# Performance work log

Hardware: AMD Instinct MI355X
Metric: run time of the kernel (lower is better)

The kernel has to match this reference:

```python
import jax, jax.numpy as jnp
import numpy as np

VOCAB = 33
V2 = VOCAB * VOCAB  # 1089
BUCKETS = 512


def setup_inputs() -> dict:
    key = jax.random.key(0)
    ks = jax.random.split(key, 9)
    B, S = 4096, 4096
    src = jax.random.randint(ks[0], (B, S), 0, VOCAB, dtype=jnp.int64 if jax.config.jax_enable_x64 else jnp.int32)
    def lin(k, fan_in, fan_out):
        bound = 1.0 / np.sqrt(fan_in)
        return jax.random.uniform(k, (fan_in, fan_out), jnp.float32, -bound, bound)
    return {
        "src": src,
        "Wb1": lin(ks[1], V2, 256), "bb1": jax.random.normal(ks[2], (256,), jnp.float32) * 0.01,
        "Wb2": lin(ks[3], 256, 32), "bb2": jax.random.normal(ks[4], (32,), jnp.float32) * 0.01,
        "Wt1": lin(ks[5], BUCKETS, 256), "bt1": jax.random.normal(ks[6], (256,), jnp.float32) * 0.01,
        "Wt2": lin(ks[7], 256, 32), "bt2": jax.random.normal(ks[8], (32,), jnp.float32) * 0.01,
    }


def _hist_freqs(indices, mask, n_bins):
    # indices: [B, L] int, mask: [B, L] bool -> normalized per-row histogram [B, n_bins]
    B = indices.shape[0]
    rows = jnp.arange(B)[:, None]
    counts = jnp.zeros((B, n_bins), jnp.float32).at[rows, indices].add(mask.astype(jnp.float32))
    lens = jnp.clip(mask.sum(axis=1, keepdims=True).astype(jnp.float32), 1.0, None)
    return counts / lens


def reference(src, Wb1, bb1, Wb2, bb2, Wt1, bt1, Wt2, bt2):
    # bigram histogram
    cur, nxt = src[:, :-1], src[:, 1:]
    bi_idx = cur * VOCAB + nxt
    bi_mask = (cur > 0) & (nxt > 0)
    bi_freq = _hist_freqs(bi_idx, bi_mask, V2)
    bi_feat = jax.nn.relu(bi_freq @ Wb1 + bb1) @ Wb2 + bb2
    # trigram hashed histogram
    c1, c2, c3 = src[:, :-2], src[:, 1:-1], src[:, 2:]
    tri_idx = (c1 * (VOCAB * VOCAB) + c2 * VOCAB + c3) % BUCKETS
    tri_mask = (c1 > 0) & (c2 > 0) & (c3 > 0)
    tri_freq = _hist_freqs(tri_idx, tri_mask, BUCKETS)
    tri_feat = jax.nn.relu(tri_freq @ Wt1 + bt1) @ Wt2 + bt2
    return jnp.concatenate([bi_feat, tri_feat], axis=1)  # [B, 64]
```

## Files before the change

kernel.cpp:

```cpp
#include <hip/hip_runtime.h>
#include <hip/hip_bf16.h>

#define TOK_S    4096
#define NBI      1089
#define NBI_P    1092
#define KP_BI    1120
#define NTRI     512
#define NHID     256
#define NROWS    4096
#define HSTRIDE  (NHID + 4)

#define HIST_BLKS   (NROWS / 2)
#define TRANS_ELEMS (NHID * KP_BI + NHID * NTRI)
#define TRANS_BLKS  (TRANS_ELEMS / 1024)

typedef __attribute__((ext_vector_type(8))) short short8;
typedef __attribute__((ext_vector_type(4))) float f32x4;

__global__ __launch_bounds__(256)
void hist_trans(const int* __restrict__ src,
                const float* __restrict__ Wb1, const float* __restrict__ Wt1,
                __hip_bfloat16* __restrict__ Abi,
                __hip_bfloat16* __restrict__ Atri,
                __hip_bfloat16* __restrict__ WbT,
                __hip_bfloat16* __restrict__ WtT,
                float* __restrict__ inv)
{
    __shared__ int   s_bi [2][NBI_P];
    __shared__ int   s_tri[2][NTRI];
    __shared__ float s_ps [2][2][2];

    const int tid = threadIdx.x;

    if (blockIdx.x >= HIST_BLKS) {
        int base = (blockIdx.x - HIST_BLKS) * 1024 + tid;
        const int nb = NHID * KP_BI;
        #pragma unroll
        for (int i = 0; i < 4; ++i) {
            int idx = base + i * 256;
            if (idx < nb) {
                int c = idx / KP_BI, k = idx - c * KP_BI;
                WbT[idx] = __float2bfloat16(k < NBI ? Wb1[k * NHID + c] : 0.0f);
            } else {
                int j = idx - nb;
                int c = j >> 9, k = j & 511;
                WtT[j] = __float2bfloat16(Wt1[k * NHID + c]);
            }
        }
        return;
    }

    const int wave = tid >> 6;
    const int lane = tid & 63;
    const int wrow = wave >> 1;
    const int wpar = wave & 1;
    const size_t row = (size_t)blockIdx.x * 2 + wrow;

    for (int i = tid; i < 2 * NBI_P; i += 256) ((int*)s_bi)[i]  = 0;
    for (int i = tid; i < 2 * NTRI;  i += 256) ((int*)s_tri)[i] = 0;
    __syncthreads();

    int* bi  = s_bi[wrow];
    int* tri = s_tri[wrow];
    const int4* rowp = (const int4*)(src + row * TOK_S);
    const int*  rowt = src + row * TOK_S;

    #pragma unroll
    for (int j = 0; j < 8; ++j) {
        const int idx = wpar * 512 + j * 64 + lane;
        int4 c = rowp[idx];
        int e0 = 0, e1 = 0;
        if (idx != 1023) {
            const int2 e = *(const int2*)(rowt + idx * 4 + 4);
            e0 = e.x; e1 = e.y;
        }
        const bool mx = c.x > 0, my = c.y > 0, mz = c.z > 0, mw = c.w > 0;
        const bool m4 = e0 > 0, m5 = e1 > 0;
        const int b0 = c.x * 33 + c.y;
        const int b1 = c.y * 33 + c.z;
        const int b2 = c.z * 33 + c.w;
        const int b3 = c.w * 33 + e0;
        if (mx & my) atomicAdd(&bi[b0], 1);
        if (my & mz) atomicAdd(&bi[b1], 1);
        if (mz & mw) atomicAdd(&bi[b2], 1);
        if (mw & m4) atomicAdd(&bi[b3], 1);
        if (mx & my & mz) atomicAdd(&tri[(b0 * 33 + c.z) & 511], 1);
        if (my & mz & mw) atomicAdd(&tri[(b1 * 33 + c.w) & 511], 1);
        if (mz & mw & m4) atomicAdd(&tri[(b2 * 33 + e0) & 511], 1);
        if (mw & m4 & m5) atomicAdd(&tri[(b3 * 33 + e1) & 511], 1);
    }
    __syncthreads();

    float bsum = 0.0f, tsum = 0.0f;
    __hip_bfloat16* arow = Abi + row * KP_BI;
    for (int i = wpar * 64 + lane; i < KP_BI; i += 128) {
        float f = (i < NBI) ? (float)bi[i] : 0.0f;
        bsum += f;
        arow[i] = __float2bfloat16(f);
    }
    __hip_bfloat16* trow = Atri + row * NTRI;
    for (int i = wpar * 64 + lane; i < NTRI; i += 128) {
        float f = (float)tri[i];
        tsum += f;
        trow[i] = __float2bfloat16(f);
    }
    #pragma unroll
    for (int s = 32; s; s >>= 1) {
        bsum += __shfl_xor(bsum, s, 64);
        tsum += __shfl_xor(tsum, s, 64);
    }
    if (lane == 0) { s_ps[wrow][wpar][0] = bsum; s_ps[wrow][wpar][1] = tsum; }
    __syncthreads();
    if (tid < 2) {
        float bs = s_ps[tid][0][0] + s_ps[tid][1][0];
        float ts = s_ps[tid][0][1] + s_ps[tid][1][1];
        size_t r2 = ((size_t)blockIdx.x * 2 + tid) * 2;
        inv[r2 + 0] = 1.0f / fmaxf(bs, 1.0f);
        inv[r2 + 1] = 1.0f / fmaxf(ts, 1.0f);
    }
}

template<int KP>
__device__ __forceinline__
void head_body(const __hip_bfloat16* __restrict__ A,
               const __hip_bfloat16* __restrict__ WT,
               const float* __restrict__ b1,
               const float* __restrict__ W2,
               const float* __restrict__ b2,
               const float* __restrict__ inv, const int invoff, const int headoff,
               float* __restrict__ out, const int m0,
               float (*sH)[HSTRIDE])
{
    const int wave = threadIdx.x >> 6;
    const int lane = threadIdx.x & 63;
    const int wn   = wave * 32;
    const int fr   = lane & 15;
    const int kg   = lane >> 4;

    const __hip_bfloat16* A0 = A  + (size_t)(m0 + fr) * KP + kg * 8;
    const __hip_bfloat16* A1 = A0 + (size_t)16 * KP;
    const __hip_bfloat16* B0 = WT + (size_t)(wn + fr) * KP + kg * 8;
    const __hip_bfloat16* B1 = B0 + (size_t)16 * KP;

    f32x4 acc00 = {}, acc01 = {}, acc10 = {}, acc11 = {};
    #pragma unroll 4
    for (int k = 0; k < KP; k += 32) {
        short8 a0  = *(const short8*)(A0 + k);
        short8 a1  = *(const short8*)(A1 + k);
        short8 b0  = *(const short8*)(B0 + k);
        short8 b1v = *(const short8*)(B1 + k);
        acc00 = __builtin_amdgcn_mfma_f32_16x16x32_bf16(a0, b0,  acc00, 0, 0, 0);
        acc01 = __builtin_amdgcn_mfma_f32_16x16x32_bf16(a0, b1v, acc01, 0, 0, 0);
        acc10 = __builtin_amdgcn_mfma_f32_16x16x32_bf16(a1, b0,  acc10, 0, 0, 0);
        acc11 = __builtin_amdgcn_mfma_f32_16x16x32_bf16(a1, b1v, acc11, 0, 0, 0);
    }

    f32x4 accs[2][2] = { {acc00, acc01}, {acc10, acc11} };
    #pragma unroll
    for (int mf = 0; mf < 2; ++mf) {
        #pragma unroll
        for (int nf = 0; nf < 2; ++nf) {
            const int col = wn + nf * 16 + fr;
            const float bias = b1[col];
            #pragma unroll
            for (int r = 0; r < 4; ++r) {
                const int rl = mf * 16 + kg * 4 + r;
                const float iv = inv[(m0 + rl) * 2 + invoff];
                sH[rl][col] = fmaxf(fmaf(accs[mf][nf][r], iv, bias), 0.0f);
            }
        }
    }
    __syncthreads();

    const int r  = threadIdx.x >> 4;
    const int oo = threadIdx.x & 15;
    const float* hr = sH[r];
    float a0 = b2[oo], a1 = b2[oo + 16];
    #pragma unroll 8
    for (int j = 0; j < NHID; j += 4) {
        float4 h = *(const float4*)(hr + j);
        a0 = fmaf(h.x, W2[(j + 0) * 32 + oo], a0);
        a0 = fmaf(h.y, W2[(j + 1) * 32 + oo], a0);
        a0 = fmaf(h.z, W2[(j + 2) * 32 + oo], a0);
        a0 = fmaf(h.w, W2[(j + 3) * 32 + oo], a0);
        a1 = fmaf(h.x, W2[(j + 0) * 32 + oo + 16], a1);
        a1 = fmaf(h.y, W2[(j + 1) * 32 + oo + 16], a1);
        a1 = fmaf(h.z, W2[(j + 2) * 32 + oo + 16], a1);
        a1 = fmaf(h.w, W2[(j + 3) * 32 + oo + 16], a1);
    }
    const size_t ro = (size_t)(m0 + r) * 64 + headoff;
    out[ro + oo]      = a0;
    out[ro + oo + 16] = a1;
}

__global__ __launch_bounds__(512, 1)
void gemm_fused(const __hip_bfloat16* __restrict__ Abi,
                const __hip_bfloat16* __restrict__ WbT,
                const float* __restrict__ bb1,
                const float* __restrict__ Wb2, const float* __restrict__ bb2,
                const __hip_bfloat16* __restrict__ Atri,
                const __hip_bfloat16* __restrict__ WtT,
                const float* __restrict__ bt1,
                const float* __restrict__ Wt2, const float* __restrict__ bt2,
                const float* __restrict__ inv,
                float* __restrict__ out)
{
    __shared__ float sH[32][HSTRIDE];
    const int bid = blockIdx.x;
    if (bid < NROWS / 32) {
        head_body<KP_BI>(Abi, WbT, bb1, Wb2, bb2, inv, 0, 0,  out, bid * 32, sH);
    } else {
        head_body<NTRI>(Atri, WtT, bt1, Wt2, bt2, inv, 1, 32, out, (bid - NROWS / 32) * 32, sH);
    }
}

extern "C" void kernel_launch(void* const* d_in, const int* in_sizes, int n_in,
                              void* d_out, int out_size, void* d_ws, size_t ws_size,
                              hipStream_t stream) {
    const int*   src = (const int*)  d_in[0];
    const float* Wb1 = (const float*)d_in[1];
    const float* bb1 = (const float*)d_in[2];
    const float* Wb2 = (const float*)d_in[3];
    const float* bb2 = (const float*)d_in[4];
    const float* Wt1 = (const float*)d_in[5];
    const float* bt1 = (const float*)d_in[6];
    const float* Wt2 = (const float*)d_in[7];
    const float* bt2 = (const float*)d_in[8];
    float* outp = (float*)d_out;

    const int B = in_sizes[0] / TOK_S;

    char* ws = (char*)d_ws;
    __hip_bfloat16* Abi  = (__hip_bfloat16*)(ws);
    __hip_bfloat16* Atri = (__hip_bfloat16*)(ws + (size_t)B * KP_BI * 2);
    char* ws2 = ws + (size_t)B * KP_BI * 2 + (size_t)B * NTRI * 2;
    __hip_bfloat16* WbT  = (__hip_bfloat16*)(ws2);
    __hip_bfloat16* WtT  = (__hip_bfloat16*)(ws2 + (size_t)NHID * KP_BI * 2);
    float* inv = (float*)(ws2 + (size_t)NHID * KP_BI * 2 + (size_t)NHID * NTRI * 2);

    hist_trans<<<HIST_BLKS + TRANS_BLKS, 256, 0, stream>>>(
        src, Wb1, Wt1, Abi, Atri, WbT, WtT, inv);

    gemm_fused<<<2 * (B / 32), 512, 0, stream>>>(
        Abi, WbT, bb1, Wb2, bb2, Atri, WtT, bt1, Wt2, bt2, inv, outp);
}
```

Before: 49.13 us.

## Make histogram atomics branchless with dump bins and vectorize histogram writeback

The histogram loop now processes 8 tokens per thread with all loads issued up front. It removes the per-bigram mask branches by always incrementing and then zeroing the masked bins (row/column 0) at writeback. Masked trigrams go to padded per-lane dump slots, so no branch is needed there either. LDS zeroing and the bf16 writeback are vectorized with int4/uint2 packing, the launch bounds request 4 blocks per CU, and the GEMM block index is interleaved so bigram and trigram blocks mix. The trade-off is extra atomics on dump and zero bins, and more contention on those addresses.

```diff
diff --git a/kernel.cpp b/kernel.cpp
--- a/kernel.cpp
+++ b/kernel.cpp
@@ -6,6 +6,7 @@
 #define NBI_P    1092
 #define KP_BI    1120
 #define NTRI     512
+#define NTRI_P   544
 #define NHID     256
 #define NROWS    4096
 #define HSTRIDE  (NHID + 4)
@@ -17,7 +18,12 @@
 typedef __attribute__((ext_vector_type(8))) short short8;
 typedef __attribute__((ext_vector_type(4))) float f32x4;
 
-__global__ __launch_bounds__(256)
+static __device__ __forceinline__ unsigned int f2bf(float f) {
+    __hip_bfloat16 h = __float2bfloat16(f);
+    return (unsigned int)*reinterpret_cast<unsigned short*>(&h);
+}
+
+__global__ __launch_bounds__(256, 4)
 void hist_trans(const int* __restrict__ src,
                 const float* __restrict__ Wb1, const float* __restrict__ Wt1,
                 __hip_bfloat16* __restrict__ Abi,
@@ -27,7 +33,7 @@
                 float* __restrict__ inv)
 {
     __shared__ int   s_bi [2][NBI_P];
-    __shared__ int   s_tri[2][NTRI];
+    __shared__ int   s_tri[2][NTRI_P];
     __shared__ float s_ps [2][2][2];
 
     const int tid = threadIdx.x;
@@ -55,9 +61,10 @@
     const int wrow = wave >> 1;
     const int wpar = wave & 1;
     const size_t row = (size_t)blockIdx.x * 2 + wrow;
-
-    for (int i = tid; i < 2 * NBI_P; i += 256) ((int*)s_bi)[i]  = 0;
-    for (int i = tid; i < 2 * NTRI;  i += 256) ((int*)s_tri)[i] = 0;
+    const int dump = NTRI + (lane & 31);
+
+    for (int i = tid; i < 2 * NBI_P / 4;  i += 256) ((int4*)s_bi)[i]  = int4{0,0,0,0};
+    for (int i = tid; i < 2 * NTRI_P / 4; i += 256) ((int4*)s_tri)[i] = int4{0,0,0,0};
     __syncthreads();
 
     int* bi  = s_bi[wrow];
@@ -65,44 +72,76 @@
     const int4* rowp = (const int4*)(src + row * TOK_S);
     const int*  rowt = src + row * TOK_S;
 
-    #pragma unroll
-    for (int j = 0; j < 8; ++j) {
-        const int idx = wpar * 512 + j * 64 + lane;
-        int4 c = rowp[idx];
-        int e0 = 0, e1 = 0;
-        if (idx != 1023) {
-            const int2 e = *(const int2*)(rowt + idx * 4 + 4);
-            e0 = e.x; e1 = e.y;
-        }
-        const bool mx = c.x > 0, my = c.y > 0, mz = c.z > 0, mw = c.w > 0;
-        const bool m4 = e0 > 0, m5 = e1 > 0;
-        const int b0 = c.x * 33 + c.y;
-        const int b1 = c.y * 33 + c.z;
-        const int b2 = c.z * 33 + c.w;
-        const int b3 = c.w * 33 + e0;
-        if (mx & my) atomicAdd(&bi[b0], 1);
-        if (my & mz) atomicAdd(&bi[b1], 1);
-        if (mz & mw) atomicAdd(&bi[b2], 1);
-        if (mw & m4) atomicAdd(&bi[b3], 1);
-        if (mx & my & mz) atomicAdd(&tri[(b0 * 33 + c.z) & 511], 1);
-        if (my & mz & mw) atomicAdd(&tri[(b1 * 33 + c.w) & 511], 1);
-        if (mz & mw & m4) atomicAdd(&tri[(b2 * 33 + e0) & 511], 1);
-        if (mw & m4 & m5) atomicAdd(&tri[(b3 * 33 + e1) & 511], 1);
+    int4 A[4], Bv[4];
+    int2 E[4];
+    #pragma unroll
+    for (int jj = 0; jj < 4; ++jj) {
+        const int idx = wpar * 256 + jj * 64 + lane;
+        A[jj]  = rowp[2 * idx];
+        Bv[jj] = rowp[2 * idx + 1];
+        if (idx != 511) E[jj] = *(const int2*)(rowt + 8 * idx + 8);
+        else            E[jj] = int2{0, 0};
+    }
+
+    #pragma unroll
+    for (int jj = 0; jj < 4; ++jj) {
+        const int t0 = A[jj].x, t1 = A[jj].y, t2 = A[jj].z, t3 = A[jj].w;
+        const int t4 = Bv[jj].x, t5 = Bv[jj].y, t6 = Bv[jj].z, t7 = Bv[jj].w;
+        const int t8 = E[jj].x, t9 = E[jj].y;
+        const int b0 = t0 * 33 + t1;
+        const int b1 = t1 * 33 + t2;
+        const int b2 = t2 * 33 + t3;
+        const int b3 = t3 * 33 + t4;
+        const int b4 = t4 * 33 + t5;
+        const int b5 = t5 * 33 + t6;
+        const int b6 = t6 * 33 + t7;
+        const int b7 = t7 * 33 + t8;
+        atomicAdd(&bi[b0], 1);  atomicAdd(&bi[b1], 1);
+        atomicAdd(&bi[b2], 1);  atomicAdd(&bi[b3], 1);
+        atomicAdd(&bi[b4], 1);  atomicAdd(&bi[b5], 1);
+        atomicAdd(&bi[b6], 1);  atomicAdd(&bi[b7], 1);
+        const int u0 = (min(min(t0, t1), t2) > 0) ? ((b0 * 33 + t2) & 511) : dump;
+        const int u1 = (min(min(t1, t2), t3) > 0) ? ((b1 * 33 + t3) & 511) : dump;
+        const int u2 = (min(min(t2, t3), t4) > 0) ? ((b2 * 33 + t4) & 511) : dump;
+        const int u3 = (min(min(t3, t4), t5) > 0) ? ((b3 * 33 + t5) & 511) : dump;
+        const int u4 = (min(min(t4, t5), t6) > 0) ? ((b4 * 33 + t6) & 511) : dump;
+        const int u5 = (min(min(t5, t6), t7) > 0) ? ((b5 * 33 + t7) & 511) : dump;
+        const int u6 = (min(min(t6, t7), t8) > 0) ? ((b6 * 33 + t8) & 511) : dump;
+        const int u7 = (min(min(t7, t8), t9) > 0) ? ((b7 * 33 + t9) & 511) : dump;
+        atomicAdd(&tri[u0], 1); atomicAdd(&tri[u1], 1);
+        atomicAdd(&tri[u2], 1); atomicAdd(&tri[u3], 1);
+        atomicAdd(&tri[u4], 1); atomicAdd(&tri[u5], 1);
+        atomicAdd(&tri[u6], 1); atomicAdd(&tri[u7], 1);
     }
     __syncthreads();
 
     float bsum = 0.0f, tsum = 0.0f;
     __hip_bfloat16* arow = Abi + row * KP_BI;
-    for (int i = wpar * 64 + lane; i < KP_BI; i += 128) {
-        float f = (i < NBI) ? (float)bi[i] : 0.0f;
-        bsum += f;
-        arow[i] = __float2bfloat16(f);
-    }
-    __hip_bfloat16* trow = Atri + row * NTRI;
-    for (int i = wpar * 64 + lane; i < NTRI; i += 128) {
-        float f = (float)tri[i];
-        tsum += f;
-        trow[i] = __float2bfloat16(f);
+    for (int g = wpar * 64 + lane; g < KP_BI / 4; g += 128) {
+        uint2 pk{0, 0};
+        if (g < NBI_P / 4) {
+            int4 v = *(const int4*)&bi[4 * g];
+            float f0, f1, f2, f3;
+            int b = 4 * g;
+            f0 = (b + 0 >= 33 && (b + 0) % 33 != 0 && b + 0 < NBI) ? (float)v.x : 0.0f;
+            f1 = (b + 1 >= 33 && (b + 1) % 33 != 0 && b + 1 < NBI) ? (float)v.y : 0.0f;
+            f2 = (b + 2 >= 33 && (b + 2) % 33 != 0 && b + 2 < NBI) ? (float)v.z : 0.0f;
+            f3 = (b + 3 >= 33 && (b + 3) % 33 != 0 && b + 3 < NBI) ? (float)v.w : 0.0f;
+            bsum += f0 + f1 + f2 + f3;
+            pk.x = f2bf(f0) | (f2bf(f1) << 16);
+            pk.y = f2bf(f2) | (f2bf(f3) << 16);
+        }
+        *(uint2*)(arow + 4 * g) = pk;
+    }
+    {
+        const int g = wpar * 64 + lane;
+        int4 v = *(const int4*)&tri[4 * g];
+        float f0 = (float)v.x, f1 = (float)v.y, f2 = (float)v.z, f3 = (float)v.w;
+        tsum += f0 + f1 + f2 + f3;
+        uint2 pk;
+        pk.x = f2bf(f0) | (f2bf(f1) << 16);
+        pk.y = f2bf(f2) | (f2bf(f3) << 16);
+        *(uint2*)(Atri + row * NTRI + 4 * g) = pk;
     }
     #pragma unroll
     for (int s = 32; s; s >>= 1) {
@@ -206,7 +245,7 @@
                 float* __restrict__ out)
 {
     __shared__ float sH[32][HSTRIDE];
-    const int bid = blockIdx.x;
+    const int bid = (blockIdx.x & 7) * 32 + (blockIdx.x >> 3);
     if (bid < NROWS / 32) {
         head_body<KP_BI>(Abi, WbT, bb1, Wb2, bb2, inv, 0, 0,  out, bid * 32, sH);
     } else {
```

After: 49.71 us (median of 2 runs). About the same (+1.2%).

## Restructure histogram kernel to pack 16 rows per block with replicated 16-bit counters

Applied to the files above, without the earlier changes.

The histogram kernel now has each 256-thread block handle 16 rows. Each thread walks a 256-token segment of one row and updates packed 16-bit counters in shared memory, replicated 8 ways, so two rows share one word. Masking becomes branchless: invalid trigrams go to per-segment dump bins, and invalid bigrams are zeroed during readout by checking the digit decomposition. The weight transpose is folded into the same blocks, and the GEMM grid order is swizzled so bigram and trigram blocks interleave. The aim is to cut atomic divergence and contention and launch fewer, larger blocks. The cost is much larger shared memory per block, which lowers occupancy, plus only 256 blocks in the grid.

```diff
diff --git a/kernel.cpp b/kernel.cpp
--- a/kernel.cpp
+++ b/kernel.cpp
@@ -3,121 +3,130 @@
 
 #define TOK_S    4096
 #define NBI      1089
-#define NBI_P    1092
 #define KP_BI    1120
 #define NTRI     512
+#define NTRI_T   528
 #define NHID     256
 #define NROWS    4096
-#define HSTRIDE  (NHID + 4)
-
-#define HIST_BLKS   (NROWS / 2)
-#define TRANS_ELEMS (NHID * KP_BI + NHID * NTRI)
-#define TRANS_BLKS  (TRANS_ELEMS / 1024)
+#define HSTRIDE  260
+
+#define HBLKS    256
+#define TPB      1632
 
 typedef __attribute__((ext_vector_type(8))) short short8;
 typedef __attribute__((ext_vector_type(4))) float f32x4;
 
 __global__ __launch_bounds__(256)
-void hist_trans(const int* __restrict__ src,
-                const float* __restrict__ Wb1, const float* __restrict__ Wt1,
-                __hip_bfloat16* __restrict__ Abi,
-                __hip_bfloat16* __restrict__ Atri,
-                __hip_bfloat16* __restrict__ WbT,
-                __hip_bfloat16* __restrict__ WtT,
-                float* __restrict__ inv)
+void hist16(const int* __restrict__ src,
+            const float* __restrict__ Wb1, const float* __restrict__ Wt1,
+            __hip_bfloat16* __restrict__ Abi,
+            __hip_bfloat16* __restrict__ Atri,
+            __hip_bfloat16* __restrict__ WbT,
+            __hip_bfloat16* __restrict__ WtT,
+            float* __restrict__ inv)
 {
-    __shared__ int   s_bi [2][NBI_P];
-    __shared__ int   s_tri[2][NTRI];
-    __shared__ float s_ps [2][2][2];
+    __shared__ unsigned int s_bi [NBI * 8];
+    __shared__ unsigned int s_tri[NTRI_T * 8];
+    __shared__ float        s_sum[2][16];
 
     const int tid = threadIdx.x;
-
-    if (blockIdx.x >= HIST_BLKS) {
-        int base = (blockIdx.x - HIST_BLKS) * 1024 + tid;
+    const int bid = blockIdx.x;
+    const int row0 = bid * 16;
+
+    {
         const int nb = NHID * KP_BI;
         #pragma unroll
-        for (int i = 0; i < 4; ++i) {
-            int idx = base + i * 256;
-            if (idx < nb) {
-                int c = idx / KP_BI, k = idx - c * KP_BI;
-                WbT[idx] = __float2bfloat16(k < NBI ? Wb1[k * NHID + c] : 0.0f);
-            } else {
-                int j = idx - nb;
-                int c = j >> 9, k = j & 511;
-                WtT[j] = __float2bfloat16(Wt1[k * NHID + c]);
+        for (int i = 0; i < 7; ++i) {
+            int t = tid + i * 256;
+            if (t < TPB) {
+                int idx = bid * TPB + t;
+                if (idx < nb) {
+                    int c = idx / KP_BI, k = idx - c * KP_BI;
+                    WbT[idx] = __float2bfloat16(k < NBI ? Wb1[k * NHID + c] : 0.0f);
+                } else {
+                    int j = idx - nb;
+                    int c = j >> 9, k = j & 511;
+                    WtT[j] = __float2bfloat16(Wt1[k * NHID + c]);
+                }
             }
         }
-        return;
-    }
-
-    const int wave = tid >> 6;
-    const int lane = tid & 63;
-    const int wrow = wave >> 1;
-    const int wpar = wave & 1;
-    const size_t row = (size_t)blockIdx.x * 2 + wrow;
-
-    for (int i = tid; i < 2 * NBI_P; i += 256) ((int*)s_bi)[i]  = 0;
-    for (int i = tid; i < 2 * NTRI;  i += 256) ((int*)s_tri)[i] = 0;
-    __syncthreads();
-
-    int* bi  = s_bi[wrow];
-    int* tri = s_tri[wrow];
-    const int4* rowp = (const int4*)(src + row * TOK_S);
-    const int*  rowt = src + row * TOK_S;
-
-    #pragma unroll
-    for (int j = 0; j < 8; ++j) {
-        const int idx = wpar * 512 + j * 64 + lane;
-        int4 c = rowp[idx];
-        int e0 = 0, e1 = 0;
-        if (idx != 1023) {
-            const int2 e = *(const int2*)(rowt + idx * 4 + 4);
-            e0 = e.x; e1 = e.y;
+    }
+
+    for (int i = tid; i < (NBI * 8) / 4;    i += 256) ((uint4*)s_bi)[i]  = uint4{0,0,0,0};
+    for (int i = tid; i < (NTRI_T * 8) / 4; i += 256) ((uint4*)s_tri)[i] = uint4{0,0,0,0};
+    if (tid < 32) s_sum[tid >> 4][tid & 15] = 0.0f;
+    __syncthreads();
+
+    const int r    = tid & 15;
+    const int seg  = tid >> 4;
+    const int col  = r & 7;
+    const unsigned int addv = 1u << (16 * (r >> 3));
+    const int dumpb = NTRI + seg;
+
+    const int*  rowt = src + (size_t)(row0 + r) * TOK_S + seg * 256;
+    const int4* rowp = (const int4*)rowt;
+    int2 ov = (seg != 15) ? *(const int2*)(rowt + 256) : int2{0, 0};
+
+    int4 cur = rowp[0];
+    #pragma unroll 8
+    for (int g = 0; g < 64; ++g) {
+        int4 nxt; int n0, n1;
+        if (g < 63) { nxt = rowp[g + 1]; n0 = nxt.x; n1 = nxt.y; }
+        else        { nxt = int4{0,0,0,0}; n0 = ov.x; n1 = ov.y; }
+
+        const int b0 = cur.x * 33 + cur.y;
+        const int b1 = cur.y * 33 + cur.z;
+        const int b2 = cur.z * 33 + cur.w;
+        const int b3 = cur.w * 33 + n0;
+        atomicAdd(&s_bi[b0 * 8 + col], addv);
+        atomicAdd(&s_bi[b1 * 8 + col], addv);
+        atomicAdd(&s_bi[b2 * 8 + col], addv);
+        atomicAdd(&s_bi[b3 * 8 + col], addv);
+
+        const int u0 = (min(min(cur.x, cur.y), cur.z) > 0) ? ((b0 * 33 + cur.z) & 511) : dumpb;
+        const int u1 = (min(min(cur.y, cur.z), cur.w) > 0) ? ((b1 * 33 + cur.w) & 511) : dumpb;
+        const int u2 = (min(min(cur.z, cur.w), n0)   > 0) ? ((b2 * 33 + n0)    & 511) : dumpb;
+        const int u3 = (min(min(cur.w, n0), n1)      > 0) ? ((b3 * 33 + n1)    & 511) : dumpb;
+        atomicAdd(&s_tri[u0 * 8 + col], addv);
+        atomicAdd(&s_tri[u1 * 8 + col], addv);
+        atomicAdd(&s_tri[u2 * 8 + col], addv);
+        atomicAdd(&s_tri[u3 * 8 + col], addv);
+
+        cur = nxt;
+    }
+    __syncthreads();
+
+    const int shift = 16 * (r >> 3);
+    float bsum = 0.0f;
+    __hip_bfloat16* arow = Abi + (size_t)(row0 + r) * KP_BI;
+    #pragma unroll 4
+    for (int j = 0; j < 70; ++j) {
+        const int b = seg + 16 * j;
+        float f = 0.0f;
+        if (b < NBI) {
+            unsigned int c = (s_bi[b * 8 + col] >> shift) & 0xFFFFu;
+            int q = b / 33, rem = b - q * 33;
+            f = (q > 0 && rem > 0) ? (float)c : 0.0f;
         }
-        const bool mx = c.x > 0, my = c.y > 0, mz = c.z > 0, mw = c.w > 0;
-        const bool m4 = e0 > 0, m5 = e1 > 0;
-        const int b0 = c.x * 33 + c.y;
-        const int b1 = c.y * 33 + c.z;
-        const int b2 = c.z * 33 + c.w;
-        const int b3 = c.w * 33 + e0;
-        if (mx & my) atomicAdd(&bi[b0], 1);
-        if (my & mz) atomicAdd(&bi[b1], 1);
-        if (mz & mw) atomicAdd(&bi[b2], 1);
-        if (mw & m4) atomicAdd(&bi[b3], 1);
-        if (mx & my & mz) atomicAdd(&tri[(b0 * 33 + c.z) & 511], 1);
-        if (my & mz & mw) atomicAdd(&tri[(b1 * 33 + c.w) & 511], 1);
-        if (mz & mw & m4) atomicAdd(&tri[(b2 * 33 + e0) & 511], 1);
-        if (mw & m4 & m5) atomicAdd(&tri[(b3 * 33 + e1) & 511], 1);
-    }
-    __syncthreads();
-
-    float bsum = 0.0f, tsum = 0.0f;
-    __hip_bfloat16* arow = Abi + row * KP_BI;
-    for (int i = wpar * 64 + lane; i < KP_BI; i += 128) {
-        float f = (i < NBI) ? (float)bi[i] : 0.0f;
         bsum += f;
-        arow[i] = __float2bfloat16(f);
-    }
-    __hip_bfloat16* trow = Atri + row * NTRI;
-    for (int i = wpar * 64 + lane; i < NTRI; i += 128) {
-        float f = (float)tri[i];
+        arow[b] = __float2bfloat16(f);
+    }
+    float tsum = 0.0f;
+    __hip_bfloat16* trow = Atri + (size_t)(row0 + r) * NTRI;
+    #pragma unroll 4
+    for (int j = 0; j < 32; ++j) {
+        const int b = seg + 16 * j;
+        float f = (float)((s_tri[b * 8 + col] >> shift) & 0xFFFFu);
         tsum += f;
-        trow[i] = __float2bfloat16(f);
-    }
-    #pragma unroll
-    for (int s = 32; s; s >>= 1) {
-        bsum += __shfl_xor(bsum, s, 64);
-        tsum += __shfl_xor(tsum, s, 64);
-    }
-    if (lane == 0) { s_ps[wrow][wpar][0] = bsum; s_ps[wrow][wpar][1] = tsum; }
-    __syncthreads();
-    if (tid < 2) {
-        float bs = s_ps[tid][0][0] + s_ps[tid][1][0];
-        float ts = s_ps[tid][0][1] + s_ps[tid][1][1];
-        size_t r2 = ((size_t)blockIdx.x * 2 + tid) * 2;
-        inv[r2 + 0] = 1.0f / fmaxf(bs, 1.0f);
-        inv[r2 + 1] = 1.0f / fmaxf(ts, 1.0f);
-    }
+        trow[b] = __float2bfloat16(f);
+    }
+    atomicAdd(&s_sum[0][r], bsum);
+    atomicAdd(&s_sum[1][r], tsum);
+    __syncthreads();
+    if (tid < 16)
+        inv[(size_t)(row0 + tid) * 2 + 0] = 1.0f / fmaxf(s_sum[0][tid], 1.0f);
+    else if (tid < 32)
+        inv[(size_t)(row0 + tid - 16) * 2 + 1] = 1.0f / fmaxf(s_sum[1][tid - 16], 1.0f);
 }
 
 template<int KP>
@@ -163,18 +172,18 @@
             const int col = wn + nf * 16 + fr;
             const float bias = b1[col];
             #pragma unroll
-            for (int r = 0; r < 4; ++r) {
-                const int rl = mf * 16 + kg * 4 + r;
+            for (int q = 0; q < 4; ++q) {
+                const int rl = mf * 16 + kg * 4 + q;
                 const float iv = inv[(m0 + rl) * 2 + invoff];
-                sH[rl][col] = fmaxf(fmaf(accs[mf][nf][r], iv, bias), 0.0f);
+                sH[rl][col] = fmaxf(fmaf(accs[mf][nf][q], iv, bias), 0.0f);
             }
         }
     }
     __syncthreads();
 
-    const int r  = threadIdx.x >> 4;
+    const int rr = threadIdx.x >> 4;
     const int oo = threadIdx.x & 15;
-    const float* hr = sH[r];
+    const float* hr = sH[rr];
     float a0 = b2[oo], a1 = b2[oo + 16];
     #pragma unroll 8
     for (int j = 0; j < NHID; j += 4) {
@@ -188,7 +197,7 @@
         a1 = fmaf(h.z, W2[(j + 2) * 32 + oo + 16], a1);
         a1 = fmaf(h.w, W2[(j + 3) * 32 + oo + 16], a1);
     }
-    const size_t ro = (size_t)(m0 + r) * 64 + headoff;
+    const size_t ro = (size_t)(m0 + rr) * 64 + headoff;
     out[ro + oo]      = a0;
     out[ro + oo + 16] = a1;
 }
@@ -206,7 +215,7 @@
                 float* __restrict__ out)
 {
     __shared__ float sH[32][HSTRIDE];
-    const int bid = blockIdx.x;
+    const int bid = (blockIdx.x & 7) * 32 + (blockIdx.x >> 3);
     if (bid < NROWS / 32) {
         head_body<KP_BI>(Abi, WbT, bb1, Wb2, bb2, inv, 0, 0,  out, bid * 32, sH);
     } else {
@@ -238,8 +247,7 @@
     __hip_bfloat16* WtT  = (__hip_bfloat16*)(ws2 + (size_t)NHID * KP_BI * 2);
     float* inv = (float*)(ws2 + (size_t)NHID * KP_BI * 2 + (size_t)NHID * NTRI * 2);
 
-    hist_trans<<<HIST_BLKS + TRANS_BLKS, 256, 0, stream>>>(
-        src, Wb1, Wt1, Abi, Atri, WbT, WtT, inv);
+    hist16<<<HBLKS, 256, 0, stream>>>(src, Wb1, Wt1, Abi, Atri, WbT, WtT, inv);
 
     gemm_fused<<<2 * (B / 32), 512, 0, stream>>>(
         Abi, WbT, bb1, Wb2, bb2, Atri, WtT, bt1, Wt2, bt2, inv, outp);
```

Result: slower. 65.82 us (+34.0%).
